# Kernel tuning notes

Hardware: AMD Instinct MI355X
Metric: run time of the kernel (lower is better)

Reference implementation:

```python
import jax, jax.numpy as jnp
import numpy as np

ALPHA = 0.2  # LeakyReLU slope
NEG = -1e9


def setup_inputs() -> dict:
    key = jax.random.key(0)
    k1, k2, k3, k4, k5 = jax.random.split(key, 5)
    B, N, F_IN, F_OUT, H = 8, 1024, 512, 256, 8
    x = jax.random.normal(k1, (B, N, F_IN), dtype=jnp.float32)
    adj = jax.random.randint(k2, (B, N, N), 0, 2, dtype=jnp.int32)
    W = jax.random.normal(k3, (H, F_OUT, F_IN), dtype=jnp.float32) * 0.05
    a1 = jax.random.normal(k4, (H, F_OUT), dtype=jnp.float32) * 0.05
    a2 = jax.random.normal(k5, (H, F_OUT), dtype=jnp.float32) * 0.05
    return {"x": x, "adj": adj, "W": W, "a1": a1, "a2": a2}


def _head(x, adj_zero, W, a1, a2):
    # x: (B,N,F_in), W: (F_out,F_in), a1/a2: (F_out,)
    h = jnp.einsum('bnf,of->bno', x, W)              # (B,N,F_out)
    f1 = jnp.einsum('bno,o->bn', h, a1)              # (B,N)
    f2 = jnp.einsum('bno,o->bn', h, a2)              # (B,N)
    e = f1[:, :, None] + f2[:, None, :]              # (B,N,N) broadcast add
    e = jax.nn.leaky_relu(e, negative_slope=ALPHA)
    e = jnp.where(adj_zero, NEG, e)                  # adjacency mask
    att = jax.nn.softmax(e, axis=2)
    return jnp.einsum('bnm,bmo->bno', att, h)        # (B,N,F_out)


def reference(x, adj, W, a1, a2):
    adj_zero = (adj == 0)
    # vmap over heads; sum of elu(head outputs)
    heads = jax.vmap(lambda w, u, v: _head(x, adj_zero, w, u, v))(W, a1, a2)  # (H,B,N,F_out)
    out = jnp.sum(jax.nn.elu(heads), axis=0)         # (B,N,F_out)
    return jax.nn.log_softmax(out, axis=2)
```

## Files before the change

kernel.cpp:

```cpp
#include <hip/hip_runtime.h>
#include <math.h>

#define B_    8
#define N_    1024
#define FIN   512
#define FOUT  256
#define H_    8
#define ALPHA 0.2f

#define XT (B_ * N_ * FIN)
#define WT (H_ * FOUT * FIN)

typedef short s16x8 __attribute__((ext_vector_type(8)));
typedef float f32x4 __attribute__((ext_vector_type(4)));

__device__ __forceinline__ unsigned short f2bf(float f) {
  unsigned int u = __float_as_uint(f);
  u = (u + 0x7FFFu + ((u >> 16) & 1u)) >> 16;
  return (unsigned short)u;
}

__device__ __forceinline__ unsigned int pk4_fp8(float a, float b, float c,
                                                float d) {
  int u = __builtin_amdgcn_cvt_pk_fp8_f32(a, b, 0, false);
  u = __builtin_amdgcn_cvt_pk_fp8_f32(c, d, u, true);
  return (unsigned int)u;
}

#if __has_builtin(__builtin_amdgcn_cvt_pk_f32_fp8)
#define HAVE_DEQ4 1
__device__ __forceinline__ float deq4(unsigned int u) {
  const auto a = __builtin_amdgcn_cvt_pk_f32_fp8((int)u, false);
  const auto b = __builtin_amdgcn_cvt_pk_f32_fp8((int)u, true);
  return (a[0] + a[1]) + (b[0] + b[1]);
}
#else
#define HAVE_DEQ4 0
__device__ __forceinline__ float q8e4m3(float p) {
  if (p >= 0.015625f) {
    unsigned int u = __float_as_uint(p);
    u = (u + 0x7FFFFu + ((u >> 20) & 1u)) & 0xFFF00000u;
    return __uint_as_float(u);
  }
  return (p + 16384.f) - 16384.f;
}
#endif


#define CVB  ((XT + WT) / 1024)
#define ZRB  192
#define PKB  ((B_ * N_ * 32) / 256)

__global__ __launch_bounds__(256) void prep(
    const float* __restrict__ x, const float* __restrict__ W,
    const int* __restrict__ adj, unsigned short* __restrict__ xb,
    unsigned short* __restrict__ Wb, float* __restrict__ f12,
    unsigned int* __restrict__ adjP) {
  const int blk = blockIdx.x;
  if (blk >= CVB + ZRB) {
    const int dw = (blk - CVB - ZRB) * 256 + threadIdx.x;
    const int r = dw >> 5, pd = dw & 31;
    const int q = pd >> 3, c8 = pd & 7;
    const int* ap = adj + (size_t)r * N_;
    unsigned int out = 0;
#pragma unroll
    for (int i = 0; i < 4; ++i) {
      const int jb = (c8 * 4 + i) * 32 + q * 8;
      int4 v0 = *(const int4*)(ap + jb);
      int4 v1 = *(const int4*)(ap + jb + 4);
      unsigned int byte = 0;
      byte |= (v0.x ? 1u : 0u) << 0; byte |= (v0.y ? 1u : 0u) << 1;
      byte |= (v0.z ? 1u : 0u) << 2; byte |= (v0.w ? 1u : 0u) << 3;
      byte |= (v1.x ? 1u : 0u) << 4; byte |= (v1.y ? 1u : 0u) << 5;
      byte |= (v1.z ? 1u : 0u) << 6; byte |= (v1.w ? 1u : 0u) << 7;
      out |= byte << (i * 8);
    }
    adjP[dw] = out;
    return;
  }
  if (blk >= CVB) {
    const int i = (blk - CVB) * 256 + threadIdx.x;
    ((float4*)f12)[i] = make_float4(0.f, 0.f, 0.f, 0.f);
    return;
  }
  const int i = (blk * 256 + threadIdx.x) * 4;
  const float* src;
  unsigned short* dst;
  int off;
  if (i < XT) { src = x; dst = xb; off = i; }
  else        { src = W; dst = Wb; off = i - XT; }
  float4 v = *(const float4*)(src + off);
  ushort4 s;
  s.x = f2bf(v.x); s.y = f2bf(v.y); s.z = f2bf(v.z); s.w = f2bf(v.w);
  *(ushort4*)(dst + off) = s;
}

__global__ __launch_bounds__(256) void proj_mfma(
    const unsigned short* __restrict__ xb, const unsigned short* __restrict__ Wb,
    const float* __restrict__ a1, const float* __restrict__ a2,
    unsigned char* __restrict__ htq, float* __restrict__ f1,
    float* __restrict__ f2) {
  __shared__ __align__(16) unsigned short As[128 * 64];
  __shared__ __align__(16) unsigned short Bs[64 * 64];
  const int gid = blockIdx.x;
  const int b = gid & 7;
  const int mt_ = (gid >> 3) & 7;
  const int ot_ = (gid >> 6) & 3;
  const int h = gid >> 8;
  const int hb = h * B_ + b;
  const int m0 = mt_ * 128, o0 = ot_ * 64;
  const int t = threadIdx.x, w = t >> 6, lane = t & 63;
  const int col = lane & 15, quad = lane >> 4;

  const int srow = t >> 3;
  const int sslot = t & 7;
  const int sseg = sslot ^ (srow & 7);
  const unsigned short* agp = xb + (size_t)(b * N_ + m0 + srow) * FIN + sseg * 8;
  const unsigned short* bgp = Wb + (size_t)(h * FOUT + o0 + srow) * FIN + sseg * 8;

  f32x4 acc[2][4];
  const f32x4 z4 = {0.f, 0.f, 0.f, 0.f};
#pragma unroll
  for (int mt = 0; mt < 2; ++mt)
#pragma unroll
    for (int ot = 0; ot < 4; ++ot) acc[mt][ot] = z4;

  s16x8 pa[4], pb[2];
#pragma unroll
  for (int i2 = 0; i2 < 4; ++i2) pa[i2] = *(const s16x8*)(agp + (size_t)i2 * 32 * FIN);
#pragma unroll
  for (int i2 = 0; i2 < 2; ++i2) pb[i2] = *(const s16x8*)(bgp + (size_t)i2 * 32 * FIN);

  for (int it = 0; it < FIN / 64; ++it) {
    __syncthreads();
#pragma unroll
    for (int i2 = 0; i2 < 4; ++i2)
      *(s16x8*)&As[(i2 * 32 + srow) * 64 + sslot * 8] = pa[i2];
#pragma unroll
    for (int i2 = 0; i2 < 2; ++i2)
      *(s16x8*)&Bs[(i2 * 32 + srow) * 64 + sslot * 8] = pb[i2];
    __syncthreads();
    if (it < FIN / 64 - 1) {
      const int k0 = (it + 1) * 64;
#pragma unroll
      for (int i2 = 0; i2 < 4; ++i2)
        pa[i2] = *(const s16x8*)(agp + (size_t)i2 * 32 * FIN + k0);
#pragma unroll
      for (int i2 = 0; i2 < 2; ++i2)
        pb[i2] = *(const s16x8*)(bgp + (size_t)i2 * 32 * FIN + k0);
    }
#pragma unroll
    for (int kb = 0; kb < 2; ++kb) {
      s16x8 af[2], bf[4];
#pragma unroll
      for (int mt = 0; mt < 2; ++mt) {
        const int row = w * 32 + mt * 16 + col;
        af[mt] = *(const s16x8*)&As[row * 64 + ((kb * 4 + quad) ^ (row & 7)) * 8];
      }
#pragma unroll
      for (int ot = 0; ot < 4; ++ot) {
        const int row = ot * 16 + col;
        bf[ot] = *(const s16x8*)&Bs[row * 64 + ((kb * 4 + quad) ^ (row & 7)) * 8];
      }
#pragma unroll
      for (int mt = 0; mt < 2; ++mt)
#pragma unroll
        for (int ot = 0; ot < 4; ++ot)
          acc[mt][ot] = __builtin_amdgcn_mfma_f32_16x16x32_bf16(af[mt], bf[ot],
                                                                acc[mt][ot], 0, 0, 0);
    }
  }

  const int kkw = (m0 >> 5) + w;
  float pf1[2][4] = {{0.f}}, pf2[2][4] = {{0.f}};
#pragma unroll
  for (int mt = 0; mt < 2; ++mt) {
#pragma unroll
    for (int ot = 0; ot < 4; ++ot) {
      const int o = o0 + ot * 16 + col;
      const float va1 = a1[h * FOUT + o], va2 = a2[h * FOUT + o];
      const int otg = (o0 >> 4) + ot;
      unsigned char* fb =
          htq + (((size_t)(hb * 16 + otg) * 32 + kkw) << 9);
      const unsigned int q =
          pk4_fp8(acc[mt][ot][0], acc[mt][ot][1], acc[mt][ot][2], acc[mt][ot][3]);
      *(unsigned int*)(fb + (2 * mt + (quad >> 1)) * 128 + col * 8 +
                       (quad & 1) * 4) = q;
#pragma unroll
      for (int r = 0; r < 4; ++r) {
        pf1[mt][r] += acc[mt][ot][r] * va1;
        pf2[mt][r] += acc[mt][ot][r] * va2;
      }
    }
  }
#pragma unroll
  for (int off = 1; off <= 8; off <<= 1)
#pragma unroll
    for (int mt = 0; mt < 2; ++mt)
#pragma unroll
      for (int r = 0; r < 4; ++r) {
        pf1[mt][r] += __shfl_xor(pf1[mt][r], off);
        pf2[mt][r] += __shfl_xor(pf2[mt][r], off);
      }
  if (col == 0) {
#pragma unroll
    for (int mt = 0; mt < 2; ++mt)
#pragma unroll
      for (int r = 0; r < 4; ++r) {
        const int n = m0 + w * 32 + mt * 16 + quad * 4 + r;
        atomicAdd(&f1[hb * N_ + n], pf1[mt][r]);
        atomicAdd(&f2[hb * N_ + n], pf2[mt][r]);
      }
  }
}

__global__ __launch_bounds__(256) void wgen(
    const float* __restrict__ f1, const float* __restrict__ f2,
    const unsigned int* __restrict__ adjP, unsigned char* __restrict__ wq,
    float* __restrict__ dnm) {
  const int id = blockIdx.x;
  const int b = id & 7, h = (id >> 3) & 7;
  const int rbg = (id >> 6) & 15;
  const int kkh = id >> 10;
  const int w = threadIdx.x >> 6, lane = threadIdx.x & 63;
  const int col = lane & 15, quad = lane >> 4;
  const int hb = h * B_ + b;
  const int rb = rbg * 4 + w;
  const int row = rb * 16 + col;

  const float* f2r = f2 + (size_t)hb * N_;
  float m2 = -3.0e38f;
#pragma unroll
  for (int c = 0; c < 16; ++c) m2 = fmaxf(m2, f2r[lane + c * 64]);
#pragma unroll
  for (int off = 32; off; off >>= 1) m2 = fmaxf(m2, __shfl_xor(m2, off));

  const float f1i = f1[(size_t)hb * N_ + row];
  const float tb = f1i + m2;
  const float mhat = fmaxf(tb, ALPHA * tb);

  const unsigned int* adp = adjP + ((size_t)(b * N_ + row) << 5) + quad * 8;
  const float* f2p = f2r + quad * 8;
  unsigned char* wp = wq + (((size_t)(hb * 64 + rb) * 32) << 9) + lane * 8;

  float dsum = 0.f;
#pragma unroll
  for (int k4i = 0; k4i < 4; ++k4i) {
    const int k4 = kkh * 4 + k4i;
    const unsigned int ad = adp[k4];
#pragma unroll
    for (int k2 = 0; k2 < 4; ++k2) {
      const int kk = k4 * 4 + k2;
      const unsigned int ab = (ad >> (k2 * 8)) & 0xFFu;
      const float4 fA = *(const float4*)(f2p + kk * 32);
      const float4 fB = *(const float4*)(f2p + kk * 32 + 4);
      float ex[8];
#pragma unroll
      for (int j = 0; j < 8; ++j) {
        const float fv = j < 4 ? ((const float*)&fA)[j]
                               : ((const float*)&fB)[j - 4];
        const float tt = f1i + fv;
        const float l = fmaxf(tt, ALPHA * tt);
        const float p = __expf(l - mhat);
        ex[j] = ((ab >> j) & 1u) ? p : 0.f;
      }
      const unsigned int lo = pk4_fp8(ex[0], ex[1], ex[2], ex[3]);
      const unsigned int hi = pk4_fp8(ex[4], ex[5], ex[6], ex[7]);
#if HAVE_DEQ4
      dsum += deq4(lo) + deq4(hi);
#else
#pragma unroll
      for (int j = 0; j < 8; ++j) dsum += q8e4m3(ex[j]);
#endif
      *(uint2*)(wp + kk * 512) = make_uint2(lo, hi);
    }
  }
  dsum += __shfl_xor(dsum, 16);
  dsum += __shfl_xor(dsum, 32);
  if (quad == 0) atomicAdd(&dnm[(size_t)hb * N_ + row], dsum);
}

__global__ __launch_bounds__(256, 4) void pv(
    const unsigned char* __restrict__ htq, const unsigned char* __restrict__ wq,
    const float* __restrict__ dnm, float* __restrict__ p0,
    float* __restrict__ p1, float* __restrict__ p2, float* __restrict__ p3) {
  const int id = blockIdx.x;
  const int b = id & 7;
  const int g0 = (id >> 3) & 3;
  const int oq = (id >> 5) & 3;
  const int it = id >> 7;
  const int w = threadIdx.x >> 6, lane = threadIdx.x & 63;
  const int col = lane & 15, quad = lane >> 4;
  const int rb = it * 8 + w * 2;

  float hsum[2][4][4];
#pragma unroll
  for (int g = 0; g < 2; ++g)
#pragma unroll
    for (int t = 0; t < 4; ++t)
#pragma unroll
      for (int r = 0; r < 4; ++r) hsum[g][t][r] = 0.f;

  for (int hh = 0; hh < 2; ++hh) {
    const int hb = (g0 * 2 + hh) * B_ + b;
    const unsigned char* ap =
        wq + (((size_t)(hb * 64 + rb) * 32) << 9) + lane * 8;
    const unsigned char* bp =
        htq + (((size_t)(hb * 16 + oq * 4) * 32) << 9) + lane * 8;
    const float* dr = dnm + (size_t)hb * N_ + quad * 4;
    const float4 den0 = *(const float4*)(dr + (rb + 0) * 16);
    const float4 den1 = *(const float4*)(dr + (rb + 1) * 16);

    f32x4 acc[2][4];
    const f32x4 z4 = {0.f, 0.f, 0.f, 0.f};
#pragma unroll
    for (int g = 0; g < 2; ++g)
#pragma unroll
      for (int t = 0; t < 4; ++t) acc[g][t] = z4;

    long xa0, xa1, xb0, xb1, xb2, xb3;
    long ya0, ya1, yb0, yb1, yb2, yb3;

#define LOADG(P, k)                                                         \
    do {                                                                    \
      P##a0 = *(const long*)(ap + (k) * 512);                               \
      P##a1 = *(const long*)(ap + 16384 + (k) * 512);                       \
      P##b0 = *(const long*)(bp + ((k) << 9));                              \
      P##b1 = *(const long*)(bp + ((32 + (k)) << 9));                       \
      P##b2 = *(const long*)(bp + ((64 + (k)) << 9));                       \
      P##b3 = *(const long*)(bp + ((96 + (k)) << 9));                       \
    } while (0)

#define MFMAG(P)                                                            \
    do {                                                                    \
      __builtin_amdgcn_s_setprio(1);                                        \
      acc[0][0] = __builtin_amdgcn_mfma_f32_16x16x32_fp8_fp8(P##a0, P##b0, acc[0][0], 0, 0, 0); \
      acc[1][0] = __builtin_amdgcn_mfma_f32_16x16x32_fp8_fp8(P##a1, P##b0, acc[1][0], 0, 0, 0); \
      acc[0][1] = __builtin_amdgcn_mfma_f32_16x16x32_fp8_fp8(P##a0, P##b1, acc[0][1], 0, 0, 0); \
      acc[1][1] = __builtin_amdgcn_mfma_f32_16x16x32_fp8_fp8(P##a1, P##b1, acc[1][1], 0, 0, 0); \
      acc[0][2] = __builtin_amdgcn_mfma_f32_16x16x32_fp8_fp8(P##a0, P##b2, acc[0][2], 0, 0, 0); \
      acc[1][2] = __builtin_amdgcn_mfma_f32_16x16x32_fp8_fp8(P##a1, P##b2, acc[1][2], 0, 0, 0); \
      acc[0][3] = __builtin_amdgcn_mfma_f32_16x16x32_fp8_fp8(P##a0, P##b3, acc[0][3], 0, 0, 0); \
      acc[1][3] = __builtin_amdgcn_mfma_f32_16x16x32_fp8_fp8(P##a1, P##b3, acc[1][3], 0, 0, 0); \
      __builtin_amdgcn_s_setprio(0);                                        \
    } while (0)

    LOADG(x, 0);
    LOADG(y, 1);
#pragma unroll 2
    for (int kk = 0; kk < 30; kk += 2) {
      MFMAG(x);
      LOADG(x, kk + 2);
      MFMAG(y);
      LOADG(y, kk + 3);
    }
    MFMAG(x);
    MFMAG(y);
#undef LOADG
#undef MFMAG

#pragma unroll
    for (int g = 0; g < 2; ++g)
#pragma unroll
      for (int r = 0; r < 4; ++r) {
        const float dv = (g == 0) ? (&den0.x)[r] : (&den1.x)[r];
        const float inv = 1.0f / dv;
#pragma unroll
        for (int t = 0; t < 4; ++t) {
          const float oh = acc[g][t][r] * inv;
          hsum[g][t][r] += oh > 0.f ? oh : __expf(oh) - 1.f;
        }
      }
  }

  float* pdst = (g0 == 0) ? p0 : (g0 == 1) ? p1 : (g0 == 2) ? p2 : p3;
#pragma unroll
  for (int g = 0; g < 2; ++g)
#pragma unroll
    for (int t = 0; t < 4; ++t)
#pragma unroll
      for (int r = 0; r < 4; ++r) {
        const int orow = (rb + g) * 16 + quad * 4 + r;
        pdst[(size_t)(b * N_ + orow) * FOUT + oq * 64 + t * 16 + col] =
            hsum[g][t][r];
      }
}

__global__ __launch_bounds__(256) void logsm(
    const float* __restrict__ p0, const float* __restrict__ p1,
    const float* __restrict__ p2, const float* __restrict__ p3,
    float* __restrict__ out) {
  const int row = blockIdx.x * 4 + (threadIdx.x >> 6);
  const int lane = threadIdx.x & 63;
  const size_t base = (size_t)row * FOUT;
  float v[4];
  float m = -3.0e38f;
#pragma unroll
  for (int c = 0; c < 4; ++c) {
    const size_t idx = base + c * 64 + lane;
    v[c] = p0[idx] + p1[idx] + p2[idx] + p3[idx];
    m = fmaxf(m, v[c]);
  }
#pragma unroll
  for (int off = 32; off; off >>= 1) m = fmaxf(m, __shfl_xor(m, off));
  float s = 0.f;
#pragma unroll
  for (int c = 0; c < 4; ++c) s += __expf(v[c] - m);
#pragma unroll
  for (int off = 32; off; off >>= 1) s += __shfl_xor(s, off);
  const float lg = m + logf(s);
#pragma unroll
  for (int c = 0; c < 4; ++c)
    out[base + c * 64 + lane] = v[c] - lg;
}

extern "C" void kernel_launch(void* const* d_in, const int* in_sizes, int n_in,
                              void* d_out, int out_size, void* d_ws,
                              size_t ws_size, hipStream_t stream) {
  const float* x   = (const float*)d_in[0];
  const int*   adj = (const int*)d_in[1];
  const float* W   = (const float*)d_in[2];
  const float* a1  = (const float*)d_in[3];
  const float* a2  = (const float*)d_in[4];
  float* out = (float*)d_out;

  unsigned char* htq = (unsigned char*)d_ws;
  unsigned short* xb = (unsigned short*)(htq + (size_t)H_ * B_ * FOUT * N_);
  unsigned short* Wb = xb + (size_t)XT;
  float* f1 = (float*)(Wb + (size_t)WT);
  float* f2 = f1 + (size_t)H_ * B_ * N_;
  float* dnm = f2 + (size_t)H_ * B_ * N_;
  float* part2 = dnm + (size_t)H_ * B_ * N_;
  float* part3 = part2 + (size_t)B_ * N_ * FOUT;
  unsigned int* adjP = (unsigned int*)(part3 + (size_t)B_ * N_ * FOUT);
  unsigned char* wq = (unsigned char*)(adjP + (size_t)B_ * N_ * 32);
  float* part1 = (float*)xb;

  prep<<<CVB + ZRB + PKB, 256, 0, stream>>>(x, W, adj, xb, Wb, f1, adjP);

  proj_mfma<<<2048, 256, 0, stream>>>(xb, Wb, a1, a2, htq, f1, f2);

  wgen<<<2048, 256, 0, stream>>>(f1, f2, adjP, wq, dnm);

  pv<<<1024, 256, 0, stream>>>(htq, wq, dnm, out, part1, part2, part3);

  logsm<<<(B_ * N_) / 4, 256, 0, stream>>>(out, part1, part2, part3, out);
}
```

Measured before the change: 210.5 us.

## Stage shared B tiles in LDS via async global_load_lds double buffering

In the pv kernel, all four waves of a block used to load the same B (htq) fragments straight from global memory. They now load them cooperatively into a double-buffered 32KB LDS tile using global_load_lds, with the next chunk prefetched while the current one is consumed. The goal is to cut the redundant global and L2 traffic for B across waves. The cost is extra __syncthreads barriers per chunk and LDS pressure that may reduce occupancy under launch_bounds(256,4). A fragments are still loaded from global memory, in batches of eight per chunk.

```diff
diff --git a/kernel.cpp b/kernel.cpp
--- a/kernel.cpp
+++ b/kernel.cpp
@@ -45,6 +45,12 @@
   return (p + 16384.f) - 16384.f;
 }
 #endif
+
+__device__ __forceinline__ void gload16(const void* g, void* l) {
+  __builtin_amdgcn_global_load_lds(
+      (const __attribute__((address_space(1))) unsigned int*)g,
+      (__attribute__((address_space(3))) unsigned int*)l, 16, 0, 0);
+}
 
 
 #define CVB  ((XT + WT) / 1024)
@@ -284,15 +290,26 @@
     const unsigned char* __restrict__ htq, const unsigned char* __restrict__ wq,
     const float* __restrict__ dnm, float* __restrict__ p0,
     float* __restrict__ p1, float* __restrict__ p2, float* __restrict__ p3) {
+  __shared__ __align__(16) unsigned char Bsh[2][16384];
   const int id = blockIdx.x;
   const int b = id & 7;
   const int g0 = (id >> 3) & 3;
   const int oq = (id >> 5) & 3;
   const int it = id >> 7;
-  const int w = threadIdx.x >> 6, lane = threadIdx.x & 63;
+  const int tid = threadIdx.x;
+  const int w = tid >> 6, lane = tid & 63;
   const int col = lane & 15, quad = lane >> 4;
   const int rb = it * 8 + w * 2;
 
+  const int hb0 = (g0 * 2 + 0) * B_ + b;
+  const int hb1 = (g0 * 2 + 1) * B_ + b;
+  const unsigned char* ap0 =
+      wq + (((size_t)(hb0 * 64 + rb) * 32) << 9) + lane * 8;
+  const unsigned char* ap1 =
+      wq + (((size_t)(hb1 * 64 + rb) * 32) << 9) + lane * 8;
+  const unsigned char* bp0 = htq + (((size_t)(hb0 * 16 + oq * 4) * 32) << 9);
+  const unsigned char* bp1 = htq + (((size_t)(hb1 * 16 + oq * 4) * 32) << 9);
+
   float hsum[2][4][4];
 #pragma unroll
   for (int g = 0; g < 2; ++g)
@@ -301,77 +318,87 @@
 #pragma unroll
       for (int r = 0; r < 4; ++r) hsum[g][t][r] = 0.f;
 
-  for (int hh = 0; hh < 2; ++hh) {
-    const int hb = (g0 * 2 + hh) * B_ + b;
-    const unsigned char* ap =
-        wq + (((size_t)(hb * 64 + rb) * 32) << 9) + lane * 8;
-    const unsigned char* bp =
-        htq + (((size_t)(hb * 16 + oq * 4) * 32) << 9) + lane * 8;
-    const float* dr = dnm + (size_t)hb * N_ + quad * 4;
-    const float4 den0 = *(const float4*)(dr + (rb + 0) * 16);
-    const float4 den1 = *(const float4*)(dr + (rb + 1) * 16);
-
-    f32x4 acc[2][4];
-    const f32x4 z4 = {0.f, 0.f, 0.f, 0.f};
-#pragma unroll
-    for (int g = 0; g < 2; ++g)
-#pragma unroll
-      for (int t = 0; t < 4; ++t) acc[g][t] = z4;
-
-    long xa0, xa1, xb0, xb1, xb2, xb3;
-    long ya0, ya1, yb0, yb1, yb2, yb3;
-
-#define LOADG(P, k)                                                         \
-    do {                                                                    \
-      P##a0 = *(const long*)(ap + (k) * 512);                               \
-      P##a1 = *(const long*)(ap + 16384 + (k) * 512);                       \
-      P##b0 = *(const long*)(bp + ((k) << 9));                              \
-      P##b1 = *(const long*)(bp + ((32 + (k)) << 9));                       \
-      P##b2 = *(const long*)(bp + ((64 + (k)) << 9));                       \
-      P##b3 = *(const long*)(bp + ((96 + (k)) << 9));                       \
-    } while (0)
-
-#define MFMAG(P)                                                            \
-    do {                                                                    \
-      __builtin_amdgcn_s_setprio(1);                                        \
-      acc[0][0] = __builtin_amdgcn_mfma_f32_16x16x32_fp8_fp8(P##a0, P##b0, acc[0][0], 0, 0, 0); \
-      acc[1][0] = __builtin_amdgcn_mfma_f32_16x16x32_fp8_fp8(P##a1, P##b0, acc[1][0], 0, 0, 0); \
-      acc[0][1] = __builtin_amdgcn_mfma_f32_16x16x32_fp8_fp8(P##a0, P##b1, acc[0][1], 0, 0, 0); \
-      acc[1][1] = __builtin_amdgcn_mfma_f32_16x16x32_fp8_fp8(P##a1, P##b1, acc[1][1], 0, 0, 0); \
-      acc[0][2] = __builtin_amdgcn_mfma_f32_16x16x32_fp8_fp8(P##a0, P##b2, acc[0][2], 0, 0, 0); \
-      acc[1][2] = __builtin_amdgcn_mfma_f32_16x16x32_fp8_fp8(P##a1, P##b2, acc[1][2], 0, 0, 0); \
-      acc[0][3] = __builtin_amdgcn_mfma_f32_16x16x32_fp8_fp8(P##a0, P##b3, acc[0][3], 0, 0, 0); \
-      acc[1][3] = __builtin_amdgcn_mfma_f32_16x16x32_fp8_fp8(P##a1, P##b3, acc[1][3], 0, 0, 0); \
-      __builtin_amdgcn_s_setprio(0);                                        \
-    } while (0)
-
-    LOADG(x, 0);
-    LOADG(y, 1);
-#pragma unroll 2
-    for (int kk = 0; kk < 30; kk += 2) {
-      MFMAG(x);
-      LOADG(x, kk + 2);
-      MFMAG(y);
-      LOADG(y, kk + 3);
-    }
-    MFMAG(x);
-    MFMAG(y);
-#undef LOADG
-#undef MFMAG
-
-#pragma unroll
-    for (int g = 0; g < 2; ++g)
-#pragma unroll
-      for (int r = 0; r < 4; ++r) {
-        const float dv = (g == 0) ? (&den0.x)[r] : (&den1.x)[r];
-        const float inv = 1.0f / dv;
-#pragma unroll
-        for (int t = 0; t < 4; ++t) {
-          const float oh = acc[g][t][r] * inv;
-          hsum[g][t][r] += oh > 0.f ? oh : __expf(oh) - 1.f;
+  f32x4 acc[2][4];
+  const f32x4 z4 = {0.f, 0.f, 0.f, 0.f};
+  float4 den0, den1;
+
+#define STAGE(buf, bptr, c)                                                  \
+  do {                                                                       \
+    _Pragma("unroll")                                                        \
+    for (int t = 0; t < 4; ++t)                                              \
+      gload16(bptr + t * 16384 + (c) * 4096 + tid * 16,                      \
+              &Bsh[buf][t * 4096 + tid * 16]);                               \
+  } while (0)
+
+  STAGE(0, bp0, 0);
+  __syncthreads();
+
+#pragma unroll
+  for (int cc = 0; cc < 8; ++cc) {
+    const int hh = cc >> 2;
+    const int c = cc & 3;
+    const int cur = cc & 1;
+    const unsigned char* ap = hh ? ap1 : ap0;
+
+    if (cc < 7) {
+      const unsigned char* nbp = ((cc + 1) >> 2) ? bp1 : bp0;
+      STAGE(1 - cur, nbp, (cc + 1) & 3);
+    }
+
+    if (c == 0) {
+      const float* dr = dnm + (size_t)(hh ? hb1 : hb0) * N_ + quad * 4;
+      den0 = *(const float4*)(dr + (rb + 0) * 16);
+      den1 = *(const float4*)(dr + (rb + 1) * 16);
+#pragma unroll
+      for (int g = 0; g < 2; ++g)
+#pragma unroll
+        for (int t = 0; t < 4; ++t) acc[g][t] = z4;
+    }
+
+    long A0[8], A1[8];
+#pragma unroll
+    for (int kkl = 0; kkl < 8; ++kkl) {
+      A0[kkl] = *(const long*)(ap + (size_t)(c * 8 + kkl) * 512);
+      A1[kkl] = *(const long*)(ap + 16384 + (size_t)(c * 8 + kkl) * 512);
+    }
+
+    const unsigned char* bl = &Bsh[cur][lane * 8];
+#pragma unroll
+    for (int kkl = 0; kkl < 8; ++kkl) {
+      const long b0 = *(const long*)(bl + 0 * 4096 + kkl * 512);
+      const long b1 = *(const long*)(bl + 1 * 4096 + kkl * 512);
+      const long b2 = *(const long*)(bl + 2 * 4096 + kkl * 512);
+      const long b3 = *(const long*)(bl + 3 * 4096 + kkl * 512);
+      __builtin_amdgcn_s_setprio(1);
+      acc[0][0] = __builtin_amdgcn_mfma_f32_16x16x32_fp8_fp8(A0[kkl], b0, acc[0][0], 0, 0, 0);
+      acc[1][0] = __builtin_amdgcn_mfma_f32_16x16x32_fp8_fp8(A1[kkl], b0, acc[1][0], 0, 0, 0);
+      acc[0][1] = __builtin_amdgcn_mfma_f32_16x16x32_fp8_fp8(A0[kkl], b1, acc[0][1], 0, 0, 0);
+      acc[1][1] = __builtin_amdgcn_mfma_f32_16x16x32_fp8_fp8(A1[kkl], b1, acc[1][1], 0, 0, 0);
+      acc[0][2] = __builtin_amdgcn_mfma_f32_16x16x32_fp8_fp8(A0[kkl], b2, acc[0][2], 0, 0, 0);
+      acc[1][2] = __builtin_amdgcn_mfma_f32_16x16x32_fp8_fp8(A1[kkl], b2, acc[1][2], 0, 0, 0);
+      acc[0][3] = __builtin_amdgcn_mfma_f32_16x16x32_fp8_fp8(A0[kkl], b3, acc[0][3], 0, 0, 0);
+      acc[1][3] = __builtin_amdgcn_mfma_f32_16x16x32_fp8_fp8(A1[kkl], b3, acc[1][3], 0, 0, 0);
+      __builtin_amdgcn_s_setprio(0);
+    }
+
+    if (c == 3) {
+#pragma unroll
+      for (int g = 0; g < 2; ++g)
+#pragma unroll
+        for (int r = 0; r < 4; ++r) {
+          const float dv = (g == 0) ? (&den0.x)[r] : (&den1.x)[r];
+          const float inv = 1.0f / dv;
+#pragma unroll
+          for (int t = 0; t < 4; ++t) {
+            const float oh = acc[g][t][r] * inv;
+            hsum[g][t][r] += oh > 0.f ? oh : __expf(oh) - 1.f;
+          }
         }
-      }
-  }
+    }
+
+    if (cc < 7) __syncthreads();
+  }
+#undef STAGE
 
   float* pdst = (g0 == 0) ? p0 : (g0 == 1) ? p1 : (g0 == 2) ? p2 : p3;
 #pragma unroll
```

After: 193.8 us. 1.09x faster.
